# Kernel optimization log

Hardware: AMD Instinct MI355X
Metric: run time of the kernel (lower is better)

Reference implementation:

```python
import jax, jax.numpy as jnp
import numpy as np

B, T, N, L, D, F = 8, 1024, 512, 4096, 512, 64  # batch, target, nodes, leaves, d_model, d_feature
BR = L // N  # branching factor: leaves per node


def setup_inputs() -> dict:
    key = jax.random.key(0)
    ks = jax.random.split(key, 10)
    s = 0.02
    return {
        "root": jax.random.normal(ks[0], (B, 1, F), dtype=jnp.float32),
        "node": jax.random.normal(ks[1], (B, N, D), dtype=jnp.float32),
        "leaf": jax.random.normal(ks[2], (B, L, D), dtype=jnp.float32),
        "target": jax.random.normal(ks[3], (B, T, D), dtype=jnp.float32),
        "Wq": jax.random.normal(ks[4], (D, F), dtype=jnp.float32) * s,
        "bq": jnp.zeros((F,), dtype=jnp.float32),
        "Wk": jax.random.normal(ks[5], (D, F), dtype=jnp.float32) * s,
        "bk": jnp.zeros((F,), dtype=jnp.float32),
        "Wv": jax.random.normal(ks[6], (D, F), dtype=jnp.float32) * s,
        "bv": jnp.zeros((F,), dtype=jnp.float32),
        "Wagg": jax.random.normal(ks[7], (D, 1), dtype=jnp.float32) * s,
        "bagg": jnp.zeros((1,), dtype=jnp.float32),
    }


def reference(root, node, leaf, target, Wq, bq, Wk, bk, Wv, bv, Wagg, bagg):
    # Shared DecoderLinear projections (same weights used for node and leaf).
    q = target @ Wq + bq                      # [B,T,F]
    node_k = node @ Wk + bk                   # [B,N,F]
    node_v = node @ Wv + bv                   # [B,N,F]
    leaf_k = leaf @ Wk + bk                   # [B,L,F]
    leaf_v = leaf @ Wv + bv                   # [B,L,F]

    scale = 1.0 / jnp.sqrt(jnp.asarray(F, dtype=q.dtype))
    # Dual-key attention weights (no value-matmul inside attention()).
    Aqn = jax.nn.softmax(jnp.einsum('btf,bnf->btn', q, node_k) * scale, axis=-1)  # [B,T,N]
    Aql = jax.nn.softmax(jnp.einsum('btf,blf->btl', q, leaf_k) * scale, axis=-1)  # [B,T,L]

    # Tree interpolation: each leaf mixes root, its parent node value, and itself.
    node_rep = jnp.repeat(node_v, BR, axis=1)               # [B,L,F]
    interp = (root + node_rep + leaf_v) / 3.0               # [B,L,F]

    # Upward cumulative aggregation: suffix mean along the leaf dimension.
    rev_cumsum = jnp.cumsum(interp[:, ::-1, :], axis=1)[:, ::-1, :]  # [B,L,F]
    counts = (L - jnp.arange(L)).astype(interp.dtype)[None, :, None]
    upward = rev_cumsum / counts                                     # [B,L,F]

    # Weighted aggregation: learned softmax weights over each node's leaf group.
    w = jax.nn.softmax((leaf @ Wagg + bagg).reshape(B, N, BR), axis=-1)   # [B,N,BR]
    node_hat = jnp.einsum('bnc,bncf->bnf', w, upward.reshape(B, N, BR, F))  # [B,N,F]

    # Fused cat + matmul + softmax.
    A = jnp.concatenate([Aqn, Aql], axis=-1)          # [B,T,N+L]
    V = jnp.concatenate([node_hat, leaf_v], axis=-2)  # [B,N+L,F]
    return jax.nn.softmax(jnp.einsum('btm,bmf->btf', A, V), axis=-1)  # [B,T,F]
```

## Files before the change

### kernel.cpp

```cpp
#include <hip/hip_runtime.h>

#define B_ 8
#define T_ 1024
#define N_ 512
#define L_ 4096
#define D_ 512
#define F_ 64
#define SLICES 4
#define TPS 18
#define KSTR 72
#define XSTR 520

typedef __attribute__((ext_vector_type(8))) short short8;
typedef __attribute__((ext_vector_type(4))) float f32x4;

__device__ __forceinline__ unsigned short f2bf(float x){
    unsigned u = __builtin_bit_cast(unsigned, x);
    u += 0x7FFFu + ((u >> 16) & 1u);
    return (unsigned short)(u >> 16);
}
__device__ __forceinline__ unsigned pack_bf(float lo, float hi){
    return (unsigned)f2bf(lo) | ((unsigned)f2bf(hi) << 16);
}
__device__ __forceinline__ float bf2f(short s){
    return __builtin_bit_cast(float, ((unsigned)(unsigned short)s) << 16);
}
__device__ __forceinline__ short8 frag_from4(unsigned d0, unsigned d1, unsigned d2, unsigned d3){
    union { unsigned u[4]; short8 s; } t;
    t.u[0] = d0; t.u[1] = d1; t.u[2] = d2; t.u[3] = d3;
    return t.s;
}

__global__ __launch_bounds__(64)
void prep_kernel(const float* __restrict__ Wq, const float* __restrict__ bq,
                 const float* __restrict__ Wk, const float* __restrict__ bk,
                 const float* __restrict__ Wv, const float* __restrict__ bv,
                 unsigned short* __restrict__ Wq_t, unsigned short* __restrict__ Wkv_t,
                 float* __restrict__ bq_s, float* __restrict__ bkv)
{
    const int n = blockIdx.x;
    const int lane = threadIdx.x;
    if (n == 192) {
        bq_s[lane]   = bq[lane] * 0.125f;
        bkv[lane]    = bk[lane];
        bkv[64+lane] = bv[lane];
        return;
    }
    const int d0 = lane * 8;
    unsigned short t[8];
    if (n < 64) {
        #pragma unroll
        for (int j = 0; j < 8; ++j) t[j] = f2bf(Wq[(size_t)(d0+j)*F_ + n] * 0.125f);
        *(uint4*)&Wq_t[(size_t)n*D_ + d0] = make_uint4(
            (unsigned)t[0]|((unsigned)t[1]<<16), (unsigned)t[2]|((unsigned)t[3]<<16),
            (unsigned)t[4]|((unsigned)t[5]<<16), (unsigned)t[6]|((unsigned)t[7]<<16));
    } else {
        const int nn  = n - 64;
        const float* W = (nn < 64) ? Wk : Wv;
        const int col = nn & 63;
        #pragma unroll
        for (int j = 0; j < 8; ++j) t[j] = f2bf(W[(size_t)(d0+j)*F_ + col]);
        *(uint4*)&Wkv_t[(size_t)nn*D_ + d0] = make_uint4(
            (unsigned)t[0]|((unsigned)t[1]<<16), (unsigned)t[2]|((unsigned)t[3]<<16),
            (unsigned)t[4]|((unsigned)t[5]<<16), (unsigned)t[6]|((unsigned)t[7]<<16));
    }
}

template<int MODE>
__global__ __launch_bounds__(256, 2)
void proj_gemm(const float* __restrict__ X,
               const unsigned short* __restrict__ Wt,
               const float* __restrict__ bias,
               const float* __restrict__ Wagg,
               const float* __restrict__ bagg,
               unsigned short* __restrict__ outK,
               float* __restrict__ outVf,
               unsigned short* __restrict__ outVt,
               float* __restrict__ outAgg)
{
    constexpr int NPW = (MODE == 0) ? 1 : 2;
    __shared__ unsigned short Xs[64 * XSTR];
    __shared__ unsigned short Vt_lds[(MODE == 2) ? (64*72) : 4];

    const int tid = threadIdx.x;
    const int r0  = blockIdx.x * 64;
    const int w = tid >> 6, l = tid & 63, c = l & 15, h = l >> 4;

    short8 breg[NPW][16];
    #pragma unroll
    for (int p = 0; p < NPW; ++p) {
        const unsigned short* wrow = Wt + (size_t)(16*(NPW*w + p) + c)*D_ + 8*h;
        #pragma unroll
        for (int kk = 0; kk < 16; ++kk)
            breg[p][kk] = *(const short8*)(wrow + kk*32);
    }

    const float4* xsrc = (const float4*)(X + (size_t)r0 * D_);
    #pragma unroll 4
    for (int j = 0; j < 32; ++j) {
        const int s = tid + j * 256;
        const float4 v = xsrc[s];
        *(uint2*)&Xs[(s >> 7)*XSTR + (s & 127)*4] =
            make_uint2(pack_bf(v.x, v.y), pack_bf(v.z, v.w));
    }
    __syncthreads();

    f32x4 acc[NPW][4];
    #pragma unroll
    for (int p = 0; p < NPW; ++p)
        #pragma unroll
        for (int m = 0; m < 4; ++m) acc[p][m] = (f32x4){0,0,0,0};

    #pragma unroll
    for (int kk = 0; kk < 16; ++kk) {
        #pragma unroll
        for (int m = 0; m < 4; ++m) {
            const short8 af = *(const short8*)&Xs[(16*m + c)*XSTR + kk*32 + 8*h];
            #pragma unroll
            for (int p = 0; p < NPW; ++p)
                acc[p][m] = __builtin_amdgcn_mfma_f32_16x16x32_bf16(af, breg[p][kk], acc[p][m], 0,0,0);
        }
    }

    #pragma unroll
    for (int p = 0; p < NPW; ++p) {
        const int s2g = NPW*w + p;
        const float bc = bias[16*s2g + c];
        if (MODE == 0 || s2g < 4) {
            #pragma unroll
            for (int m = 0; m < 4; ++m)
                #pragma unroll
                for (int r = 0; r < 4; ++r)
                    outK[(size_t)(r0 + 16*m + 4*h + r)*F_ + 16*s2g + c] = f2bf(acc[p][m][r] + bc);
        } else if (MODE == 1) {
            #pragma unroll
            for (int m = 0; m < 4; ++m)
                #pragma unroll
                for (int r = 0; r < 4; ++r)
                    outVf[(size_t)(r0 + 16*m + 4*h + r)*F_ + 16*(s2g-4) + c] = acc[p][m][r] + bc;
        } else {
            #pragma unroll
            for (int m = 0; m < 4; ++m)
                #pragma unroll
                for (int r = 0; r < 4; ++r)
                    Vt_lds[(16*(s2g-4) + c)*72 + 16*m + 4*h + r] = f2bf(acc[p][m][r] + bc);
        }
    }

    if constexpr (MODE == 2) {
        {
            const int row = tid >> 2, qd = tid & 3;
            const unsigned short* xr = &Xs[row*XSTR + qd*128];
            const float* wr = Wagg + qd*128;
            float p = 0.f;
            #pragma unroll
            for (int j = 0; j < 16; ++j) {
                const short8 xv = *(const short8*)(xr + j*8);
                const float4 wa0 = *(const float4*)(wr + j*8);
                const float4 wa1 = *(const float4*)(wr + j*8 + 4);
                p += bf2f(xv[0])*wa0.x + bf2f(xv[1])*wa0.y
                   + bf2f(xv[2])*wa0.z + bf2f(xv[3])*wa0.w
                   + bf2f(xv[4])*wa1.x + bf2f(xv[5])*wa1.y
                   + bf2f(xv[6])*wa1.z + bf2f(xv[7])*wa1.w;
            }
            p += __shfl_xor(p, 1);
            p += __shfl_xor(p, 2);
            if (qd == 0) outAgg[r0 + row] = p + bagg[0];
        }
        __syncthreads();
        {
            const int f = tid >> 2, seg = tid & 3;
            const int b = r0 >> 12, l0 = r0 & (L_ - 1);
            const uint4 a0 = *(const uint4*)&Vt_lds[f*72 + seg*16];
            const uint4 a1 = *(const uint4*)&Vt_lds[f*72 + seg*16 + 8];
            unsigned short* dst = outVt + ((size_t)(b*F_ + f))*L_ + l0 + seg*16;
            *(uint4*)dst = a0;
            *(uint4*)(dst + 8) = a1;
        }
    }
}

__global__ __launch_bounds__(256)
void scan_kernel(const unsigned short* __restrict__ lvt,
                 const float* __restrict__ node_v,
                 const float* __restrict__ root,
                 float* __restrict__ Tnext)
{
    const int gtid = blockIdx.x * 256 + threadIdx.x;
    const int wv   = gtid >> 6;
    const int lane = threadIdx.x & 63;
    const int b = wv >> 6;
    const int f = wv & 63;

    const unsigned short* vt = lvt + ((size_t)(b*F_ + f))*L_ + lane*64;
    const float rootf = root[b*F_ + f];
    float gv[8];
    #pragma unroll
    for (int g = 0; g < 8; ++g) {
        const short8 xv = *(const short8*)(vt + g*8);
        const float s8 = bf2f(xv[0])+bf2f(xv[1])+bf2f(xv[2])+bf2f(xv[3])
                       + bf2f(xv[4])+bf2f(xv[5])+bf2f(xv[6])+bf2f(xv[7]);
        const float nv = node_v[((size_t)(b*N_ + lane*8 + g))*F_ + f];
        gv[g] = (s8 + 8.f*(rootf + nv)) * (1.f/3.f);
    }

    float s[9];
    s[8] = 0.f;
    #pragma unroll
    for (int j = 7; j >= 0; --j) s[j] = s[j+1] + gv[j];

    float x = s[0];
    const float lsum = x;
    #pragma unroll
    for (int off = 1; off < 64; off <<= 1) {
        float t = __shfl_down(x, off);
        if (lane + off < 64) x += t;
    }
    const float excl = x - lsum;

    float* outp = Tnext + ((size_t)(b*N_ + lane*8))*F_ + f;
    #pragma unroll
    for (int j = 0; j < 8; ++j) outp[(size_t)j*F_] = excl + s[j+1];
}

__global__ __launch_bounds__(64)
void node_hat_kernel(const float* __restrict__ Tnext, const float* __restrict__ agg,
                     const unsigned short* __restrict__ lvt, const float* __restrict__ node_v,
                     const float* __restrict__ root, unsigned short* __restrict__ nh_t)
{
    const int bn = blockIdx.x;
    const int b = bn >> 9;
    const int n = bn & (N_ - 1);
    const int f = threadIdx.x;

    float a[8];
    #pragma unroll
    for (int c = 0; c < 8; ++c) a[c] = agg[(size_t)b*L_ + n*8 + c];
    float mx = a[0];
    #pragma unroll
    for (int c = 1; c < 8; ++c) mx = fmaxf(mx, a[c]);
    float wgt[8]; float wsum = 0.f;
    #pragma unroll
    for (int c = 0; c < 8; ++c) { wgt[c] = __expf(a[c] - mx); wsum += wgt[c]; }

    const float tn    = Tnext[(size_t)bn*F_ + f];
    const float rootf = root[b*F_ + f];
    const float nv    = node_v[(size_t)bn*F_ + f];
    const short8 lv8  = *(const short8*)(lvt + ((size_t)(b*F_ + f))*L_ + n*8);
    float run = 0.f, acc = 0.f;
    #pragma unroll
    for (int c = 7; c >= 0; --c) {
        const int l = n*8 + c;
        const float interp = (rootf + nv + bf2f(lv8[c])) * (1.f/3.f);
        run += interp;
        const float up = (tn + run) / (float)(L_ - l);
        acc = fmaf(wgt[c], up, acc);
    }
    nh_t[((size_t)(b*F_ + f))*N_ + n] = f2bf(acc / wsum);
}

__global__ __launch_bounds__(512, 4)
void attn_kernel(const unsigned short* __restrict__ qb,
                 const unsigned short* __restrict__ nk,
                 const unsigned short* __restrict__ nht,
                 const unsigned short* __restrict__ lk,
                 const unsigned short* __restrict__ lvt,
                 float* __restrict__ pacc, float* __restrict__ pd)
{
    __shared__ unsigned short Ks[2][64*KSTR];
    __shared__ unsigned short Vt[2][64*KSTR];

    const int wg  = (blockIdx.x & 7) * 32 + (blockIdx.x >> 3);
    const int b   = wg >> 5;
    const int sl  = (wg >> 3) & 3;
    const int t0  = (wg & 7) * 128;

    const int tid = threadIdx.x;
    const int w   = tid >> 6;
    const int l   = tid & 63;
    const int c   = l & 15;
    const int h   = l >> 4;
    const int sm  = tid >> 3;
    const int sc  = tid & 7;

    const unsigned short* qrow = qb + ((size_t)(b*T_ + t0 + w*16 + c))*F_ + 8*h;
    const short8 qf0 = *(const short8*)qrow;
    const short8 qf1 = *(const short8*)(qrow + 32);

    f32x4 accN[4] = {{0,0,0,0},{0,0,0,0},{0,0,0,0},{0,0,0,0}};
    f32x4 accL[4] = {{0,0,0,0},{0,0,0,0},{0,0,0,0},{0,0,0,0}};
    float dsN = 0.f, dsL = 0.f;

    const unsigned short* Knb = nk  + (size_t)b*N_*F_;
    const unsigned short* Klb = lk  + (size_t)b*L_*F_;
    const unsigned short* Vnb = nht + (size_t)b*F_*N_;
    const unsigned short* Vlb = lvt + (size_t)b*F_*L_;

    const int ti0 = sl * TPS;

    uint4 sk0, sv0;
    auto load_tile = [&](int ti) {
        if (ti < 8) {
            sk0 = *(const uint4*)(Knb + (size_t)ti*64*F_ + sm*64 + sc*8);
            sv0 = *(const uint4*)(Vnb + (size_t)sm*N_ + ti*64 + sc*8);
        } else {
            sk0 = *(const uint4*)(Klb + (size_t)(ti-8)*64*F_ + sm*64 + sc*8);
            sv0 = *(const uint4*)(Vlb + (size_t)sm*L_ + (ti-8)*64 + sc*8);
        }
    };
    auto write_tile = [&](int pb) {
        *(uint4*)&Ks[pb][sm*KSTR + sc*8] = sk0;
        *(uint4*)&Vt[pb][sm*KSTR + sc*8] = sv0;
    };

    load_tile(ti0);
    write_tile(0);
    __syncthreads();

    const int srcA = c + 16*((2*h) & 3);
    const int srcB = c + 16*((2*h + 1) & 3);
    const int hs   = h >> 1;

    for (int i = 0; i < TPS; ++i) {
        const int  ti  = ti0 + i;
        const bool isN = ti < 8;
        const int  pb  = i & 1;
        const bool nxt = (i + 1 < TPS);
        if (nxt) load_tile(ti + 1);

        f32x4 st[4] = {{0,0,0,0},{0,0,0,0},{0,0,0,0},{0,0,0,0}};
        #pragma unroll
        for (int ss = 0; ss < 4; ++ss) {
            const short8 kf0 = *(const short8*)&Ks[pb][(16*ss + c)*KSTR + 8*h];
            st[ss] = __builtin_amdgcn_mfma_f32_16x16x32_bf16(kf0, qf0, st[ss], 0,0,0);
            const short8 kf1 = *(const short8*)&Ks[pb][(16*ss + c)*KSTR + 32 + 8*h];
            st[ss] = __builtin_amdgcn_mfma_f32_16x16x32_bf16(kf1, qf1, st[ss], 0,0,0);
        }

        unsigned pk0[4], pk1[4];
        float psum = 0.f;
        #pragma unroll
        for (int ss = 0; ss < 4; ++ss) {
            #pragma unroll
            for (int r = 0; r < 4; ++r) { st[ss][r] = __expf(st[ss][r]); psum += st[ss][r]; }
            pk0[ss] = pack_bf(st[ss][0], st[ss][1]);
            pk1[ss] = pack_bf(st[ss][2], st[ss][3]);
        }
        if (isN) dsN += psum; else dsL += psum;

        #pragma unroll
        for (int k00 = 0; k00 < 2; ++k00) {
            const unsigned d0a = __shfl(pk0[2*k00+0], srcA);
            const unsigned d0b = __shfl(pk0[2*k00+1], srcA);
            const unsigned d1a = __shfl(pk1[2*k00+0], srcA);
            const unsigned d1b = __shfl(pk1[2*k00+1], srcA);
            const unsigned d2a = __shfl(pk0[2*k00+0], srcB);
            const unsigned d2b = __shfl(pk0[2*k00+1], srcB);
            const unsigned d3a = __shfl(pk1[2*k00+0], srcB);
            const unsigned d3b = __shfl(pk1[2*k00+1], srcB);
            const short8 bp = frag_from4(hs ? d0b : d0a, hs ? d1b : d1a,
                                         hs ? d2b : d2a, hs ? d3b : d3a);
            if (isN) {
                #pragma unroll
                for (int s2 = 0; s2 < 4; ++s2) {
                    const short8 af = *(const short8*)&Vt[pb][(16*s2 + c)*KSTR + 32*k00 + 8*h];
                    accN[s2] = __builtin_amdgcn_mfma_f32_16x16x32_bf16(af, bp, accN[s2], 0,0,0);
                }
            } else {
                #pragma unroll
                for (int s2 = 0; s2 < 4; ++s2) {
                    const short8 af = *(const short8*)&Vt[pb][(16*s2 + c)*KSTR + 32*k00 + 8*h];
                    accL[s2] = __builtin_amdgcn_mfma_f32_16x16x32_bf16(af, bp, accL[s2], 0,0,0);
                }
            }
        }

        if (nxt) {
            write_tile(pb ^ 1);
            __syncthreads();
        }
    }

    dsN += __shfl_xor(dsN, 16);  dsN += __shfl_xor(dsN, 32);
    dsL += __shfl_xor(dsL, 16);  dsL += __shfl_xor(dsL, 32);

    const int gt = b*T_ + t0 + w*16 + c;
    float* baseN = pacc + (((size_t)sl*(B_*T_) + gt)*2 + 0)*F_;
    float* baseL = baseN + F_;
    #pragma unroll
    for (int s2 = 0; s2 < 4; ++s2) {
        #pragma unroll
        for (int r = 0; r < 4; ++r) {
            baseN[s2*16 + 4*h + r] = accN[s2][r];
            baseL[s2*16 + 4*h + r] = accL[s2][r];
        }
    }
    if (h == 0) {
        pd[((size_t)sl*(B_*T_) + gt)*2 + 0] = dsN;
        pd[((size_t)sl*(B_*T_) + gt)*2 + 1] = dsL;
    }
}

__global__ __launch_bounds__(256)
void combine_kernel(const float* __restrict__ pacc, const float* __restrict__ pd,
                    float* __restrict__ out)
{
    const int gt = (blockIdx.x * 256 + threadIdx.x) >> 6;
    const int f  = threadIdx.x & 63;

    float aN = 0.f, aL = 0.f, dN = 0.f, dL = 0.f;
    #pragma unroll
    for (int s = 0; s < SLICES; ++s) {
        const size_t base = ((size_t)s*(B_*T_) + gt)*2;
        aN += pacc[(base + 0)*F_ + f];
        aL += pacc[(base + 1)*F_ + f];
        dN += pd[base + 0];
        dL += pd[base + 1];
    }
    float lg = aN / dN + aL / dL;
    float mx = lg;
    #pragma unroll
    for (int off = 1; off < 64; off <<= 1) mx = fmaxf(mx, __shfl_xor(mx, off));
    const float e = __expf(lg - mx);
    float ssum = e;
    #pragma unroll
    for (int off = 1; off < 64; off <<= 1) ssum += __shfl_xor(ssum, off);
    out[(size_t)gt*F_ + f] = e / ssum;
}

extern "C" void kernel_launch(void* const* d_in, const int* in_sizes, int n_in,
                              void* d_out, int out_size, void* d_ws, size_t ws_size,
                              hipStream_t stream)
{
    const float* root   = (const float*)d_in[0];
    const float* node   = (const float*)d_in[1];
    const float* leaf   = (const float*)d_in[2];
    const float* target = (const float*)d_in[3];
    const float* Wq   = (const float*)d_in[4];
    const float* bq   = (const float*)d_in[5];
    const float* Wk   = (const float*)d_in[6];
    const float* bk   = (const float*)d_in[7];
    const float* Wv   = (const float*)d_in[8];
    const float* bv   = (const float*)d_in[9];
    const float* Wagg = (const float*)d_in[10];
    const float* bagg = (const float*)d_in[11];
    float* out = (float*)d_out;

    char* wp = (char*)d_ws;
    unsigned short* q_bf  = (unsigned short*)wp; wp += (size_t)B_*T_*F_*2;
    unsigned short* nk_bf = (unsigned short*)wp; wp += (size_t)B_*N_*F_*2;
    unsigned short* lk_bf = (unsigned short*)wp; wp += (size_t)B_*L_*F_*2;
    unsigned short* lvt   = (unsigned short*)wp; wp += (size_t)B_*F_*L_*2;
    unsigned short* nht   = (unsigned short*)wp; wp += (size_t)B_*F_*N_*2;
    unsigned short* Wq_t  = (unsigned short*)wp; wp += (size_t)64*D_*2;
    unsigned short* Wkv_t = (unsigned short*)wp; wp += (size_t)128*D_*2;
    float* node_v = (float*)wp; wp += (size_t)B_*N_*F_*4;
    float* agg    = (float*)wp; wp += (size_t)B_*L_*4;
    float* Tnext  = (float*)wp; wp += (size_t)B_*N_*F_*4;
    float* bq_s   = (float*)wp; wp += 512;
    float* bkv    = (float*)wp; wp += 512;
    float* pacc   = (float*)wp; wp += (size_t)SLICES*B_*T_*2*F_*4;
    float* pd     = (float*)wp;

    prep_kernel<<<193, 64, 0, stream>>>(Wq, bq, Wk, bk, Wv, bv, Wq_t, Wkv_t, bq_s, bkv);
    proj_gemm<0><<<(B_*T_)/64, 256, 0, stream>>>(target, Wq_t, bq_s,
        nullptr, nullptr, q_bf, nullptr, nullptr, nullptr);
    proj_gemm<1><<<(B_*N_)/64, 256, 0, stream>>>(node, Wkv_t, bkv,
        nullptr, nullptr, nk_bf, node_v, nullptr, nullptr);
    proj_gemm<2><<<(B_*L_)/64, 256, 0, stream>>>(leaf, Wkv_t, bkv,
        Wagg, bagg, lk_bf, nullptr, lvt, agg);
    scan_kernel<<<128, 256, 0, stream>>>(lvt, node_v, root, Tnext);
    node_hat_kernel<<<B_*N_, 64, 0, stream>>>(Tnext, agg, lvt, node_v, root, nht);
    attn_kernel<<<B_*(T_/128)*SLICES, 512, 0, stream>>>(q_bf, nk_bf, nht, lk_bf, lvt, pacc, pd);
    combine_kernel<<<(B_*T_)/4, 256, 0, stream>>>(pacc, pd, out);
}
```

Measured before the change: 96.66 us.

## Merge projection launches, fuse scan with node_hat, double attention slices, bf16 partials

Folds the three projection GEMMs into one launch that picks a mode from the block index, and fuses the suffix-scan and node_hat kernels so the Tnext round trip through memory goes away. Splits attention over 8 key slices instead of 4 to put more blocks in flight. Partial accumulators are now stored in bf16, which halves combine traffic but adds rounding error and doubles the number of partials to reduce.

```diff
diff --git a/kernel.cpp b/kernel.cpp
--- a/kernel.cpp
+++ b/kernel.cpp
@@ -6,8 +6,8 @@
 #define L_ 4096
 #define D_ 512
 #define F_ 64
-#define SLICES 4
-#define TPS 18
+#define SLICES 8
+#define TPS 9
 #define KSTR 72
 #define XSTR 520
 
@@ -22,8 +22,8 @@
 __device__ __forceinline__ unsigned pack_bf(float lo, float hi){
     return (unsigned)f2bf(lo) | ((unsigned)f2bf(hi) << 16);
 }
-__device__ __forceinline__ float bf2f(short s){
-    return __builtin_bit_cast(float, ((unsigned)(unsigned short)s) << 16);
+__device__ __forceinline__ float bf2f(unsigned short s){
+    return __builtin_bit_cast(float, ((unsigned)s) << 16);
 }
 __device__ __forceinline__ short8 frag_from4(unsigned d0, unsigned d1, unsigned d2, unsigned d3){
     union { unsigned u[4]; short8 s; } t;
@@ -67,23 +67,17 @@
 }
 
 template<int MODE>
-__global__ __launch_bounds__(256, 2)
-void proj_gemm(const float* __restrict__ X,
-               const unsigned short* __restrict__ Wt,
-               const float* __restrict__ bias,
-               const float* __restrict__ Wagg,
-               const float* __restrict__ bagg,
-               unsigned short* __restrict__ outK,
-               float* __restrict__ outVf,
-               unsigned short* __restrict__ outVt,
-               float* __restrict__ outAgg)
+__device__ __forceinline__ void proj_body(
+    int r0, unsigned short* Xs, unsigned short* Vt_lds,
+    const float* __restrict__ X,
+    const unsigned short* __restrict__ Wt,
+    const float* __restrict__ bias,
+    const float* __restrict__ Wagg, const float* __restrict__ bagg,
+    unsigned short* __restrict__ outK, float* __restrict__ outVf,
+    unsigned short* __restrict__ outVt, float* __restrict__ outAgg)
 {
     constexpr int NPW = (MODE == 0) ? 1 : 2;
-    __shared__ unsigned short Xs[64 * XSTR];
-    __shared__ unsigned short Vt_lds[(MODE == 2) ? (64*72) : 4];
-
     const int tid = threadIdx.x;
-    const int r0  = blockIdx.x * 64;
     const int w = tid >> 6, l = tid & 63, c = l & 15, h = l >> 4;
 
     short8 breg[NPW][16];
@@ -158,10 +152,10 @@
                 const short8 xv = *(const short8*)(xr + j*8);
                 const float4 wa0 = *(const float4*)(wr + j*8);
                 const float4 wa1 = *(const float4*)(wr + j*8 + 4);
-                p += bf2f(xv[0])*wa0.x + bf2f(xv[1])*wa0.y
-                   + bf2f(xv[2])*wa0.z + bf2f(xv[3])*wa0.w
-                   + bf2f(xv[4])*wa1.x + bf2f(xv[5])*wa1.y
-                   + bf2f(xv[6])*wa1.z + bf2f(xv[7])*wa1.w;
+                p += bf2f((unsigned short)xv[0])*wa0.x + bf2f((unsigned short)xv[1])*wa0.y
+                   + bf2f((unsigned short)xv[2])*wa0.z + bf2f((unsigned short)xv[3])*wa0.w
+                   + bf2f((unsigned short)xv[4])*wa1.x + bf2f((unsigned short)xv[5])*wa1.y
+                   + bf2f((unsigned short)xv[6])*wa1.z + bf2f((unsigned short)xv[7])*wa1.w;
             }
             p += __shfl_xor(p, 1);
             p += __shfl_xor(p, 2);
@@ -180,11 +174,38 @@
     }
 }
 
+__global__ __launch_bounds__(256, 2)
+void proj_all(const float* __restrict__ target, const float* __restrict__ node,
+              const float* __restrict__ leaf,
+              const unsigned short* __restrict__ Wq_t,
+              const unsigned short* __restrict__ Wkv_t,
+              const float* __restrict__ bq_s, const float* __restrict__ bkv,
+              const float* __restrict__ Wagg, const float* __restrict__ bagg,
+              unsigned short* __restrict__ q_bf, unsigned short* __restrict__ nk_bf,
+              float* __restrict__ node_v, unsigned short* __restrict__ lk_bf,
+              unsigned short* __restrict__ lvt, float* __restrict__ agg)
+{
+    __shared__ unsigned short Xs[64 * XSTR];
+    __shared__ unsigned short Vt_lds[64 * 72];
+    const int blk = blockIdx.x;
+    if (blk < 512) {
+        proj_body<2>(blk*64, Xs, Vt_lds, leaf, Wkv_t, bkv, Wagg, bagg,
+                     lk_bf, nullptr, lvt, agg);
+    } else if (blk < 640) {
+        proj_body<0>((blk-512)*64, Xs, Vt_lds, target, Wq_t, bq_s, nullptr, nullptr,
+                     q_bf, nullptr, nullptr, nullptr);
+    } else {
+        proj_body<1>((blk-640)*64, Xs, Vt_lds, node, Wkv_t, bkv, nullptr, nullptr,
+                     nk_bf, node_v, nullptr, nullptr);
+    }
+}
+
 __global__ __launch_bounds__(256)
-void scan_kernel(const unsigned short* __restrict__ lvt,
-                 const float* __restrict__ node_v,
-                 const float* __restrict__ root,
-                 float* __restrict__ Tnext)
+void scan_nh_kernel(const unsigned short* __restrict__ lvt,
+                    const float* __restrict__ node_v,
+                    const float* __restrict__ root,
+                    const float* __restrict__ agg,
+                    unsigned short* __restrict__ nh_t)
 {
     const int gtid = blockIdx.x * 256 + threadIdx.x;
     const int wv   = gtid >> 6;
@@ -194,14 +215,15 @@
 
     const unsigned short* vt = lvt + ((size_t)(b*F_ + f))*L_ + lane*64;
     const float rootf = root[b*F_ + f];
-    float gv[8];
+    short8 xv[8]; float nv[8]; float gv[8];
     #pragma unroll
     for (int g = 0; g < 8; ++g) {
-        const short8 xv = *(const short8*)(vt + g*8);
-        const float s8 = bf2f(xv[0])+bf2f(xv[1])+bf2f(xv[2])+bf2f(xv[3])
-                       + bf2f(xv[4])+bf2f(xv[5])+bf2f(xv[6])+bf2f(xv[7]);
-        const float nv = node_v[((size_t)(b*N_ + lane*8 + g))*F_ + f];
-        gv[g] = (s8 + 8.f*(rootf + nv)) * (1.f/3.f);
+        xv[g] = *(const short8*)(vt + g*8);
+        nv[g] = node_v[((size_t)(b*N_ + lane*8 + g))*F_ + f];
+        float s8 = 0.f;
+        #pragma unroll
+        for (int j = 0; j < 8; ++j) s8 += bf2f((unsigned short)xv[g][j]);
+        gv[g] = (s8 + 8.f*(rootf + nv[g])) * (1.f/3.f);
     }
 
     float s[9];
@@ -218,45 +240,33 @@
     }
     const float excl = x - lsum;
 
-    float* outp = Tnext + ((size_t)(b*N_ + lane*8))*F_ + f;
-    #pragma unroll
-    for (int j = 0; j < 8; ++j) outp[(size_t)j*F_] = excl + s[j+1];
-}
-
-__global__ __launch_bounds__(64)
-void node_hat_kernel(const float* __restrict__ Tnext, const float* __restrict__ agg,
-                     const unsigned short* __restrict__ lvt, const float* __restrict__ node_v,
-                     const float* __restrict__ root, unsigned short* __restrict__ nh_t)
-{
-    const int bn = blockIdx.x;
-    const int b = bn >> 9;
-    const int n = bn & (N_ - 1);
-    const int f = threadIdx.x;
-
-    float a[8];
-    #pragma unroll
-    for (int c = 0; c < 8; ++c) a[c] = agg[(size_t)b*L_ + n*8 + c];
-    float mx = a[0];
-    #pragma unroll
-    for (int c = 1; c < 8; ++c) mx = fmaxf(mx, a[c]);
-    float wgt[8]; float wsum = 0.f;
-    #pragma unroll
-    for (int c = 0; c < 8; ++c) { wgt[c] = __expf(a[c] - mx); wsum += wgt[c]; }
-
-    const float tn    = Tnext[(size_t)bn*F_ + f];
-    const float rootf = root[b*F_ + f];
-    const float nv    = node_v[(size_t)bn*F_ + f];
-    const short8 lv8  = *(const short8*)(lvt + ((size_t)(b*F_ + f))*L_ + n*8);
-    float run = 0.f, acc = 0.f;
-    #pragma unroll
-    for (int c = 7; c >= 0; --c) {
-        const int l = n*8 + c;
-        const float interp = (rootf + nv + bf2f(lv8[c])) * (1.f/3.f);
-        run += interp;
-        const float up = (tn + run) / (float)(L_ - l);
-        acc = fmaf(wgt[c], up, acc);
-    }
-    nh_t[((size_t)(b*F_ + f))*N_ + n] = f2bf(acc / wsum);
+    const float* aggb = agg + (size_t)b*L_ + lane*64;
+    unsigned short out8[8];
+    #pragma unroll
+    for (int g = 0; g < 8; ++g) {
+        const float4 a0 = *(const float4*)(aggb + g*8);
+        const float4 a1 = *(const float4*)(aggb + g*8 + 4);
+        const float av[8] = {a0.x,a0.y,a0.z,a0.w, a1.x,a1.y,a1.z,a1.w};
+        float mx = av[0];
+        #pragma unroll
+        for (int cc = 1; cc < 8; ++cc) mx = fmaxf(mx, av[cc]);
+        float wgt[8]; float wsum = 0.f;
+        #pragma unroll
+        for (int cc = 0; cc < 8; ++cc) { wgt[cc] = __expf(av[cc] - mx); wsum += wgt[cc]; }
+
+        const float tn = excl + s[g+1];
+        float run = 0.f, acc = 0.f;
+        #pragma unroll
+        for (int cc = 7; cc >= 0; --cc) {
+            const int ll = lane*64 + g*8 + cc;
+            const float interp = (rootf + nv[g] + bf2f((unsigned short)xv[g][cc])) * (1.f/3.f);
+            run += interp;
+            const float up = (tn + run) / (float)(L_ - ll);
+            acc = fmaf(wgt[cc], up, acc);
+        }
+        out8[g] = f2bf(acc / wsum);
+    }
+    *(uint4*)&nh_t[((size_t)(b*F_ + f))*N_ + lane*8] = *(const uint4*)out8;
 }
 
 __global__ __launch_bounds__(512, 4)
@@ -265,14 +275,14 @@
                  const unsigned short* __restrict__ nht,
                  const unsigned short* __restrict__ lk,
                  const unsigned short* __restrict__ lvt,
-                 float* __restrict__ pacc, float* __restrict__ pd)
+                 unsigned short* __restrict__ pacc, float* __restrict__ pd)
 {
     __shared__ unsigned short Ks[2][64*KSTR];
     __shared__ unsigned short Vt[2][64*KSTR];
 
-    const int wg  = (blockIdx.x & 7) * 32 + (blockIdx.x >> 3);
-    const int b   = wg >> 5;
-    const int sl  = (wg >> 3) & 3;
+    const int wg  = (blockIdx.x & 7) * 64 + (blockIdx.x >> 3);
+    const int b   = wg >> 6;
+    const int sl  = (wg >> 3) & 7;
     const int t0  = (wg & 7) * 128;
 
     const int tid = threadIdx.x;
@@ -385,15 +395,14 @@
     dsL += __shfl_xor(dsL, 16);  dsL += __shfl_xor(dsL, 32);
 
     const int gt = b*T_ + t0 + w*16 + c;
-    float* baseN = pacc + (((size_t)sl*(B_*T_) + gt)*2 + 0)*F_;
-    float* baseL = baseN + F_;
+    unsigned short* baseN = pacc + (((size_t)sl*(B_*T_) + gt)*2 + 0)*F_;
+    unsigned short* baseL = baseN + F_;
     #pragma unroll
     for (int s2 = 0; s2 < 4; ++s2) {
-        #pragma unroll
-        for (int r = 0; r < 4; ++r) {
-            baseN[s2*16 + 4*h + r] = accN[s2][r];
-            baseL[s2*16 + 4*h + r] = accL[s2][r];
-        }
+        *(unsigned*)&baseN[s2*16 + 4*h]     = pack_bf(accN[s2][0], accN[s2][1]);
+        *(unsigned*)&baseN[s2*16 + 4*h + 2] = pack_bf(accN[s2][2], accN[s2][3]);
+        *(unsigned*)&baseL[s2*16 + 4*h]     = pack_bf(accL[s2][0], accL[s2][1]);
+        *(unsigned*)&baseL[s2*16 + 4*h + 2] = pack_bf(accL[s2][2], accL[s2][3]);
     }
     if (h == 0) {
         pd[((size_t)sl*(B_*T_) + gt)*2 + 0] = dsN;
@@ -402,7 +411,8 @@
 }
 
 __global__ __launch_bounds__(256)
-void combine_kernel(const float* __restrict__ pacc, const float* __restrict__ pd,
+void combine_kernel(const unsigned short* __restrict__ pacc,
+                    const float* __restrict__ pd,
                     float* __restrict__ out)
 {
     const int gt = (blockIdx.x * 256 + threadIdx.x) >> 6;
@@ -412,8 +422,8 @@
     #pragma unroll
     for (int s = 0; s < SLICES; ++s) {
         const size_t base = ((size_t)s*(B_*T_) + gt)*2;
-        aN += pacc[(base + 0)*F_ + f];
-        aL += pacc[(base + 1)*F_ + f];
+        aN += bf2f(pacc[(base + 0)*F_ + f]);
+        aL += bf2f(pacc[(base + 1)*F_ + f]);
         dN += pd[base + 0];
         dL += pd[base + 1];
     }
@@ -456,21 +466,15 @@
     unsigned short* Wkv_t = (unsigned short*)wp; wp += (size_t)128*D_*2;
     float* node_v = (float*)wp; wp += (size_t)B_*N_*F_*4;
     float* agg    = (float*)wp; wp += (size_t)B_*L_*4;
-    float* Tnext  = (float*)wp; wp += (size_t)B_*N_*F_*4;
     float* bq_s   = (float*)wp; wp += 512;
     float* bkv    = (float*)wp; wp += 512;
-    float* pacc   = (float*)wp; wp += (size_t)SLICES*B_*T_*2*F_*4;
+    unsigned short* pacc = (unsigned short*)wp; wp += (size_t)SLICES*B_*T_*2*F_*2;
     float* pd     = (float*)wp;
 
     prep_kernel<<<193, 64, 0, stream>>>(Wq, bq, Wk, bk, Wv, bv, Wq_t, Wkv_t, bq_s, bkv);
-    proj_gemm<0><<<(B_*T_)/64, 256, 0, stream>>>(target, Wq_t, bq_s,
-        nullptr, nullptr, q_bf, nullptr, nullptr, nullptr);
-    proj_gemm<1><<<(B_*N_)/64, 256, 0, stream>>>(node, Wkv_t, bkv,
-        nullptr, nullptr, nk_bf, node_v, nullptr, nullptr);
-    proj_gemm<2><<<(B_*L_)/64, 256, 0, stream>>>(leaf, Wkv_t, bkv,
-        Wagg, bagg, lk_bf, nullptr, lvt, agg);
-    scan_kernel<<<128, 256, 0, stream>>>(lvt, node_v, root, Tnext);
-    node_hat_kernel<<<B_*N_, 64, 0, stream>>>(Tnext, agg, lvt, node_v, root, nht);
+    proj_all<<<704, 256, 0, stream>>>(target, node, leaf, Wq_t, Wkv_t, bq_s, bkv,
+                                      Wagg, bagg, q_bf, nk_bf, node_v, lk_bf, lvt, agg);
+    scan_nh_kernel<<<128, 256, 0, stream>>>(lvt, node_v, root, agg, nht);
     attn_kernel<<<B_*(T_/128)*SLICES, 512, 0, stream>>>(q_bf, nk_bf, nht, lk_bf, lvt, pacc, pd);
     combine_kernel<<<(B_*T_)/4, 256, 0, stream>>>(pacc, pd, out);
 }
```

Result: faster. 80.79 us (median of 2 runs) (-16.4%).
